# Kernel optimization log

Hardware: AMD Instinct MI355X
Metric: run time of the kernel (lower is better)

The kernel has to match this reference:

```python
import jax, jax.numpy as jnp
import numpy as np

NUM_CLASSES = 10
LAMBDA_COORD = 5.0
LAMBDA_NOOBJ = 0.5
B, S, P = 2048, 26, 5 + NUM_CLASSES


def setup_inputs() -> dict:
    key = jax.random.key(0)
    k1, k2 = jax.random.split(key)
    predictions = jax.random.normal(k1, (B, S, S, P), dtype=jnp.float32)
    targets = jax.random.normal(k2, (B, S * S * P,), dtype=jnp.float32)
    return {"predictions": predictions, "targets": targets}


def reference(predictions, targets):
    b, s, _, p = predictions.shape
    pred = predictions.reshape(b, s * s, p)          # (B, S*S, 5+C)
    tgt = targets.reshape(b, s * s, -1)              # (B, S*S, 5+C)

    obj = tgt[..., 4] > 0                            # object mask per cell

    # Coordinate loss: lambda_coord * sum((pred_xywh - tgt_xywh)^2) over object cells
    coord_sq = jnp.sum((pred[..., :4] - tgt[..., :4]) ** 2, axis=-1)
    coord_loss = LAMBDA_COORD * jnp.sum(jnp.where(obj, coord_sq, 0.0))

    # Confidence loss: (sigmoid(p_conf) - t_conf)^2 on obj cells,
    # lambda_noobj * sigmoid(p_conf)^2 on no-obj cells (scalar MSE mean == squared diff)
    conf_p = jax.nn.sigmoid(pred[..., 4])
    conf_loss = jnp.sum(jnp.where(obj,
                                  (conf_p - tgt[..., 4]) ** 2,
                                  LAMBDA_NOOBJ * conf_p ** 2))

    # Classification loss: mean over C of squared diff per object cell, summed
    cls_sq = jnp.mean((pred[..., 5:5 + NUM_CLASSES] - tgt[..., 5:5 + NUM_CLASSES]) ** 2, axis=-1)
    class_loss = jnp.sum(jnp.where(obj, cls_sq, 0.0))

    total_loss = coord_loss + conf_loss + class_loss
    return (total_loss, coord_loss, conf_loss, class_loss)
```

## Files before the change

kernel.cpp:

```cpp
#include <hip/hip_runtime.h>

constexpr int   NUM_CLASSES  = 10;
constexpr float LAMBDA_COORD = 5.0f;
constexpr float LAMBDA_NOOBJ = 0.5f;
constexpr int   BLOCK = 256;
constexpr int   NBLOCKS_MAX = 2028;
constexpr int   UNROLL = 5;

__device__ __forceinline__ void slot(const float4 p, const float4 t,
                                     const float t4a, const float t4b,
                                     unsigned j0,
                                     float& coord, float& conf, float& cls)
{
    const float pm[4] = {p.x, p.y, p.z, p.w};
    const float tm[4] = {t.x, t.y, t.z, t.w};

#pragma unroll
    for (int m = 0; m < 4; ++m) {
        unsigned j  = j0 + (unsigned)m;
        float d     = pm[m] - tm[m];
        float sq    = d * d;
        float t4    = (j >= 15u) ? t4b : t4a;
        float sqo   = (t4 > 0.f) ? sq : 0.f;
        coord += ((j - 4u) >= 11u) ? sqo : 0.f;
        cls   += ((j - 5u) <  10u) ? sqo : 0.f;
    }

    bool  hasConf = (j0 - 1u) < 4u;
    float pc = (j0 == 4u) ? pm[0]
             : (j0 == 3u) ? pm[1]
             : (j0 == 2u) ? pm[2]
             :              pm[3];
    float e   = __expf(-pc);
    float sig = 1.f / (1.f + e);
    bool  obj = t4a > 0.f;
    float dsv = sig - t4a;
    float confv = obj ? dsv * dsv : LAMBDA_NOOBJ * sig * sig;
    conf += hasConf ? confv : 0.f;
}

__global__ __launch_bounds__(BLOCK) void yolo_main(
    const float4* __restrict__ pred4,
    const float4* __restrict__ tgt4,
    const float*  __restrict__ tgt,
    float* __restrict__ ws,
    unsigned n4, unsigned nblocks)
{
    unsigned idx    = blockIdx.x * BLOCK + threadIdx.x;
    unsigned stride = nblocks * BLOCK;

    float coord = 0.f, conf = 0.f, cls = 0.f;

    unsigned k = idx;
    for (; k + (UNROLL - 1) * stride < n4; k += UNROLL * stride) {
        float4   p[UNROLL], t[UNROLL];
        float    ta[UNROLL], tb[UNROLL];
        unsigned j0s[UNROLL];

#pragma unroll
        for (int u = 0; u < UNROLL; ++u) {
            unsigned kk    = k + (unsigned)u * stride;
            p[u]           = pred4[kk];
            t[u]           = tgt4[kk];
            unsigned base  = 4u * kk;
            unsigned cell0 = base / 15u;
            unsigned c15   = cell0 * 15u;
            unsigned j0    = base - c15;
            j0s[u]         = j0;
            ta[u]          = tgt[c15 + 4u];
            tb[u]          = tgt[(j0 >= 12u) ? c15 + 19u : c15 + 4u];
        }

#pragma unroll
        for (int u = 0; u < UNROLL; ++u)
            slot(p[u], t[u], ta[u], tb[u], j0s[u], coord, conf, cls);
    }

    for (; k < n4; k += stride) {
        float4 p = pred4[k];
        float4 t = tgt4[k];
        unsigned base  = 4u * k;
        unsigned cell0 = base / 15u;
        unsigned c15   = cell0 * 15u;
        unsigned j0    = base - c15;
        float ta = tgt[c15 + 4u];
        float tb = tgt[(j0 >= 12u) ? c15 + 19u : c15 + 4u];
        slot(p, t, ta, tb, j0, coord, conf, cls);
    }

#pragma unroll
    for (int off = 32; off > 0; off >>= 1) {
        coord += __shfl_down(coord, off);
        conf  += __shfl_down(conf,  off);
        cls   += __shfl_down(cls,   off);
    }

    __shared__ float s[3][4];
    int wave = threadIdx.x >> 6, lane = threadIdx.x & 63;
    if (lane == 0) { s[0][wave] = coord; s[1][wave] = conf; s[2][wave] = cls; }
    __syncthreads();

    if (threadIdx.x == 0) {
        float c0 = s[0][0] + s[0][1] + s[0][2] + s[0][3];
        float c1 = s[1][0] + s[1][1] + s[1][2] + s[1][3];
        float c2 = s[2][0] + s[2][1] + s[2][2] + s[2][3];
        ws[blockIdx.x]               = c0;
        ws[nblocks + blockIdx.x]     = c1;
        ws[2 * nblocks + blockIdx.x] = c2;
    }
}

__global__ __launch_bounds__(BLOCK) void yolo_finalize(
    const float* __restrict__ ws, float* __restrict__ out, unsigned nblocks)
{
    float c0 = 0.f, c1 = 0.f, c2 = 0.f;
    for (unsigned i = threadIdx.x; i < nblocks; i += BLOCK) {
        c0 += ws[i];
        c1 += ws[nblocks + i];
        c2 += ws[2 * nblocks + i];
    }
#pragma unroll
    for (int off = 32; off > 0; off >>= 1) {
        c0 += __shfl_down(c0, off);
        c1 += __shfl_down(c1, off);
        c2 += __shfl_down(c2, off);
    }
    __shared__ float s[3][4];
    int wave = threadIdx.x >> 6, lane = threadIdx.x & 63;
    if (lane == 0) { s[0][wave] = c0; s[1][wave] = c1; s[2][wave] = c2; }
    __syncthreads();
    if (threadIdx.x == 0) {
        float coord = LAMBDA_COORD * (s[0][0] + s[0][1] + s[0][2] + s[0][3]);
        float conf  =                 s[1][0] + s[1][1] + s[1][2] + s[1][3];
        float cls   = (1.f / NUM_CLASSES) * (s[2][0] + s[2][1] + s[2][2] + s[2][3]);
        out[0] = coord + conf + cls;
        out[1] = coord;
        out[2] = conf;
        out[3] = cls;
    }
}

extern "C" void kernel_launch(void* const* d_in, const int* in_sizes, int n_in,
                              void* d_out, int out_size, void* d_ws, size_t ws_size,
                              hipStream_t stream) {
    const float* pred = (const float*)d_in[0];
    const float* tgt  = (const float*)d_in[1];
    float* out = (float*)d_out;
    float* ws  = (float*)d_ws;

    unsigned total = (unsigned)in_sizes[0];
    unsigned n4    = total / 4u;

    unsigned nblocks = NBLOCKS_MAX;
    size_t need = (size_t)nblocks * 3 * sizeof(float);
    if (need > ws_size) nblocks = (unsigned)(ws_size / (3 * sizeof(float)));

    yolo_main<<<nblocks, BLOCK, 0, stream>>>(
        (const float4*)pred, (const float4*)tgt, tgt, ws, n4, nblocks);
    yolo_finalize<<<1, BLOCK, 0, stream>>>(ws, out, nblocks);
}
```

Measured before the change: 185.0 us.

## Stage tiles through LDS with async global_load_lds double buffering

The grid-stride register-unrolled loop is replaced by a tile loop. Each block streams 256-float4 tiles of predictions and targets into LDS using global_load_lds, double-buffered so the next tile loads while the current one is computed. The per-cell objectness values come from the LDS target tile plus small halo regions, which removes the extra scattered global reads of tgt[c15+4]. The cost is a __syncthreads per tile, only one float4 in flight per thread instead of five, and more LDS use, which may reduce occupancy.

New measurement: 186.0 us. No clear change (+0.5%).

```diff
diff --git a/kernel.cpp b/kernel.cpp
--- a/kernel.cpp
+++ b/kernel.cpp
@@ -5,7 +5,15 @@
 constexpr float LAMBDA_NOOBJ = 0.5f;
 constexpr int   BLOCK = 256;
 constexpr int   NBLOCKS_MAX = 2028;
-constexpr int   UNROLL = 5;
+
+constexpr int LDSP_F  = 256 * 4;
+constexpr int LDST_F  = 12 + 1024 + 16;
+constexpr int LDST_FP = 1056;
+
+#define GLOAD_LDS16(gp, lp) \
+    __builtin_amdgcn_global_load_lds( \
+        (const __attribute__((address_space(1))) void*)(gp), \
+        (__attribute__((address_space(3))) void*)(lp), 16, 0, 0)
 
 __device__ __forceinline__ void slot(const float4 p, const float4 t,
                                      const float t4a, const float t4b,
@@ -46,46 +54,81 @@
     float* __restrict__ ws,
     unsigned n4, unsigned nblocks)
 {
-    unsigned idx    = blockIdx.x * BLOCK + threadIdx.x;
-    unsigned stride = nblocks * BLOCK;
+    __shared__ float ldsP[2][LDSP_F];
+    __shared__ float ldsT[2][LDST_FP];
+
+    const int tid = (int)threadIdx.x;
+    const unsigned ntiles = n4 / 256u;
 
     float coord = 0.f, conf = 0.f, cls = 0.f;
 
-    unsigned k = idx;
-    for (; k + (UNROLL - 1) * stride < n4; k += UNROLL * stride) {
-        float4   p[UNROLL], t[UNROLL];
-        float    ta[UNROLL], tb[UNROLL];
-        unsigned j0s[UNROLL];
-
-#pragma unroll
-        for (int u = 0; u < UNROLL; ++u) {
-            unsigned kk    = k + (unsigned)u * stride;
-            p[u]           = pred4[kk];
-            t[u]           = tgt4[kk];
-            unsigned base  = 4u * kk;
+    unsigned NT = (ntiles > blockIdx.x) ? ((ntiles - 1u - blockIdx.x) / nblocks + 1u) : 0u;
+
+    if (NT > 0) {
+        {
+            unsigned s0 = blockIdx.x * 256u;
+            GLOAD_LDS16(pred4 + s0 + tid, &ldsP[0][4 * tid]);
+            GLOAD_LDS16(tgt4  + s0 + tid, &ldsT[0][12 + 4 * tid]);
+            if (tid < 7) {
+                int hs = (tid < 3) ? (int)s0 - 3 + tid : (int)s0 + 253 + tid;
+                hs = hs < 0 ? 0 : hs;
+                hs = hs > (int)n4 - 1 ? (int)n4 - 1 : hs;
+                float4 hv = tgt4[hs];
+                int off = (tid < 3) ? 4 * tid : 1036 + 4 * (tid - 3);
+                *(float4*)&ldsT[0][off] = hv;
+            }
+        }
+        __syncthreads();
+
+        for (unsigned T = 0; T < NT; ++T) {
+            const int cur  = (int)(T & 1u);
+            const bool more = (T + 1u < NT);
+
+            float4 hv = make_float4(0.f, 0.f, 0.f, 0.f);
+            if (more) {
+                unsigned s0n = (blockIdx.x + (T + 1u) * nblocks) * 256u;
+                GLOAD_LDS16(pred4 + s0n + tid, &ldsP[cur ^ 1][4 * tid]);
+                GLOAD_LDS16(tgt4  + s0n + tid, &ldsT[cur ^ 1][12 + 4 * tid]);
+                if (tid < 7) {
+                    int hs = (tid < 3) ? (int)s0n - 3 + tid : (int)s0n + 253 + tid;
+                    hs = hs < 0 ? 0 : hs;
+                    hs = hs > (int)n4 - 1 ? (int)n4 - 1 : hs;
+                    hv = tgt4[hs];
+                }
+            }
+
+            {
+                unsigned s0   = (blockIdx.x + T * nblocks) * 256u;
+                float4 p = *(const float4*)&ldsP[cur][4 * tid];
+                float4 t = *(const float4*)&ldsT[cur][12 + 4 * tid];
+                unsigned base = (s0 + (unsigned)tid) * 4u;
+                unsigned j0   = base % 15u;
+                int qoff = 4 * tid + 16 - (int)j0;
+                float t4a = ldsT[cur][qoff];
+                float t4b = ldsT[cur][qoff + ((j0 >= 12u) ? 15 : 0)];
+                slot(p, t, t4a, t4b, j0, coord, conf, cls);
+            }
+
+            if (more && tid < 7) {
+                int off = (tid < 3) ? 4 * tid : 1036 + 4 * (tid - 3);
+                *(float4*)&ldsT[cur ^ 1][off] = hv;
+            }
+            __syncthreads();
+        }
+    }
+
+    if (blockIdx.x == 0) {
+        for (unsigned k = ntiles * 256u + (unsigned)tid; k < n4; k += BLOCK) {
+            float4 p = pred4[k];
+            float4 t = tgt4[k];
+            unsigned base  = 4u * k;
             unsigned cell0 = base / 15u;
             unsigned c15   = cell0 * 15u;
             unsigned j0    = base - c15;
-            j0s[u]         = j0;
-            ta[u]          = tgt[c15 + 4u];
-            tb[u]          = tgt[(j0 >= 12u) ? c15 + 19u : c15 + 4u];
+            float ta = tgt[c15 + 4u];
+            float tb = tgt[(j0 >= 12u) ? c15 + 19u : c15 + 4u];
+            slot(p, t, ta, tb, j0, coord, conf, cls);
         }
-
-#pragma unroll
-        for (int u = 0; u < UNROLL; ++u)
-            slot(p[u], t[u], ta[u], tb[u], j0s[u], coord, conf, cls);
-    }
-
-    for (; k < n4; k += stride) {
-        float4 p = pred4[k];
-        float4 t = tgt4[k];
-        unsigned base  = 4u * k;
-        unsigned cell0 = base / 15u;
-        unsigned c15   = cell0 * 15u;
-        unsigned j0    = base - c15;
-        float ta = tgt[c15 + 4u];
-        float tb = tgt[(j0 >= 12u) ? c15 + 19u : c15 + 4u];
-        slot(p, t, ta, tb, j0, coord, conf, cls);
     }
 
 #pragma unroll
@@ -96,11 +139,11 @@
     }
 
     __shared__ float s[3][4];
-    int wave = threadIdx.x >> 6, lane = threadIdx.x & 63;
+    int wave = tid >> 6, lane = tid & 63;
     if (lane == 0) { s[0][wave] = coord; s[1][wave] = conf; s[2][wave] = cls; }
     __syncthreads();
 
-    if (threadIdx.x == 0) {
+    if (tid == 0) {
         float c0 = s[0][0] + s[0][1] + s[0][2] + s[0][3];
         float c1 = s[1][0] + s[1][1] + s[1][2] + s[1][3];
         float c2 = s[2][0] + s[2][1] + s[2][2] + s[2][3];
```

## Stage target tiles into LDS via async global_load_lds with double buffering

Applied to the files above, without the earlier changes.

Replaces the unrolled register-load loop with a two-stage software pipeline. Each wave streams its slice of the target tensor into a per-wave LDS buffer using global_load_lds, plus a few halo float4 loads, and prediction loads are marked nontemporal. The per-cell objectness values (t4a/t4b) are then read from LDS instead of issuing extra scattered global loads. This removes the redundant gathers of the confidence column and overlaps the next tile's loads with the current tile's math. In exchange it adds manual waitcnt/sched_barrier control, halo-handling complexity and LDS usage that may limit occupancy.

Measured after the change: 179.5 us. -3.0%, faster.

```diff
diff --git a/kernel.cpp b/kernel.cpp
--- a/kernel.cpp
+++ b/kernel.cpp
@@ -1,36 +1,42 @@
 #include <hip/hip_runtime.h>
+
+typedef float f4v __attribute__((ext_vector_type(4)));
 
 constexpr int   NUM_CLASSES  = 10;
 constexpr float LAMBDA_COORD = 5.0f;
 constexpr float LAMBDA_NOOBJ = 0.5f;
 constexpr int   BLOCK = 256;
 constexpr int   NBLOCKS_MAX = 2028;
-constexpr int   UNROLL = 5;
-
-__device__ __forceinline__ void slot(const float4 p, const float4 t,
+constexpr int   LDST_W = 288;
+
+#define GLOAD_LDS16(gp, lp) \
+    __builtin_amdgcn_global_load_lds( \
+        (const __attribute__((address_space(1))) void*)(gp), \
+        (__attribute__((address_space(3))) void*)(lp), 16, 0, 0)
+#define WAITVM(n)  asm volatile("s_waitcnt vmcnt(" #n ")" ::: "memory")
+#define WAITLGKM() asm volatile("s_waitcnt lgkmcnt(0)" ::: "memory")
+#define SB()       __builtin_amdgcn_sched_barrier(0)
+
+__device__ __forceinline__ void slot(const f4v p, const f4v t,
                                      const float t4a, const float t4b,
                                      unsigned j0,
                                      float& coord, float& conf, float& cls)
 {
-    const float pm[4] = {p.x, p.y, p.z, p.w};
-    const float tm[4] = {t.x, t.y, t.z, t.w};
-
 #pragma unroll
     for (int m = 0; m < 4; ++m) {
         unsigned j  = j0 + (unsigned)m;
-        float d     = pm[m] - tm[m];
+        float d     = p[m] - t[m];
         float sq    = d * d;
         float t4    = (j >= 15u) ? t4b : t4a;
         float sqo   = (t4 > 0.f) ? sq : 0.f;
         coord += ((j - 4u) >= 11u) ? sqo : 0.f;
         cls   += ((j - 5u) <  10u) ? sqo : 0.f;
     }
-
     bool  hasConf = (j0 - 1u) < 4u;
-    float pc = (j0 == 4u) ? pm[0]
-             : (j0 == 3u) ? pm[1]
-             : (j0 == 2u) ? pm[2]
-             :              pm[3];
+    float pc = (j0 == 4u) ? p[0]
+             : (j0 == 3u) ? p[1]
+             : (j0 == 2u) ? p[2]
+             :              p[3];
     float e   = __expf(-pc);
     float sig = 1.f / (1.f + e);
     bool  obj = t4a > 0.f;
@@ -39,52 +45,102 @@
     conf += hasConf ? confv : 0.f;
 }
 
+#define STAGE(LBUF, TT, PREG, HREG) do {                                     \
+    unsigned kk_ = idx + (unsigned)(TT) * S;                                 \
+    PREG = __builtin_nontemporal_load((const f4v*)pred4 + kk_);              \
+    GLOAD_LDS16((const f4v*)tgt4 + kk_, (LBUF) + 12 + 4 * lane);             \
+    if (lane < 7u) {                                                         \
+        int kw_ = (int)(kk_ - lane);                                         \
+        int hs_ = (lane < 3u) ? kw_ - 3 + (int)lane : kw_ + 61 + (int)lane;  \
+        hs_ = hs_ < 0 ? 0 : hs_;                                             \
+        hs_ = hs_ > (int)n4 - 1 ? (int)n4 - 1 : hs_;                         \
+        HREG = *((const f4v*)tgt4 + hs_);                                    \
+    }                                                                        \
+} while (0)
+
+#define CLOAD(LBUF, TT, HREG, TV, AV, BV, JV) do {                           \
+    if (lane < 7u) {                                                         \
+        int off_ = (lane < 3u) ? 4 * (int)lane : 268 + 4 * ((int)lane - 3);  \
+        *(f4v*)((LBUF) + off_) = HREG;                                       \
+    }                                                                        \
+    unsigned kk_ = idx + (unsigned)(TT) * S;                                 \
+    JV = (4u * kk_) % 15u;                                                   \
+    int q_ = 4 * (int)lane + 16 - (int)JV;                                   \
+    TV = *(const f4v*)((LBUF) + 12 + 4 * lane);                              \
+    AV = (LBUF)[q_];                                                         \
+    BV = (LBUF)[q_ + ((JV >= 12u) ? 15 : 0)];                                \
+} while (0)
+
 __global__ __launch_bounds__(BLOCK) void yolo_main(
-    const float4* __restrict__ pred4,
-    const float4* __restrict__ tgt4,
-    const float*  __restrict__ tgt,
+    const float* __restrict__ pred4,
+    const float* __restrict__ tgt4,
     float* __restrict__ ws,
     unsigned n4, unsigned nblocks)
 {
-    unsigned idx    = blockIdx.x * BLOCK + threadIdx.x;
-    unsigned stride = nblocks * BLOCK;
+    __shared__ float ldsT[4][2][LDST_W];
+
+    const unsigned tid  = threadIdx.x;
+    const unsigned lane = tid & 63u;
+    const unsigned wv   = tid >> 6;
+    const unsigned S    = nblocks * 256u;
+    const unsigned idx  = blockIdx.x * 256u + tid;
+    const unsigned NTu  = n4 / S;
+
+    float* L0 = &ldsT[wv][0][0];
+    float* L1 = &ldsT[wv][1][0];
 
     float coord = 0.f, conf = 0.f, cls = 0.f;
-
-    unsigned k = idx;
-    for (; k + (UNROLL - 1) * stride < n4; k += UNROLL * stride) {
-        float4   p[UNROLL], t[UNROLL];
-        float    ta[UNROLL], tb[UNROLL];
-        unsigned j0s[UNROLL];
-
-#pragma unroll
-        for (int u = 0; u < UNROLL; ++u) {
-            unsigned kk    = k + (unsigned)u * stride;
-            p[u]           = pred4[kk];
-            t[u]           = tgt4[kk];
-            unsigned base  = 4u * kk;
-            unsigned cell0 = base / 15u;
-            unsigned c15   = cell0 * 15u;
-            unsigned j0    = base - c15;
-            j0s[u]         = j0;
-            ta[u]          = tgt[c15 + 4u];
-            tb[u]          = tgt[(j0 >= 12u) ? c15 + 19u : c15 + 4u];
+    f4v pA = {0,0,0,0}, pB = {0,0,0,0}, hA = {0,0,0,0}, hB = {0,0,0,0};
+
+    if (NTu >= 2u) {
+        STAGE(L0, 0, pA, hA); SB();
+        STAGE(L1, 1, pB, hB); SB();
+        unsigned T = 0;
+        for (; T + 1u < NTu; T += 2u) {
+            WAITVM(3); SB();
+            f4v tA; float aA, bA; unsigned jA;
+            CLOAD(L0, T, hA, tA, aA, bA, jA);
+            WAITLGKM(); SB();
+            f4v puA = pA;
+            if (T + 2u < NTu) { STAGE(L0, T + 2u, pA, hA); }
+            SB();
+            slot(puA, tA, aA, bA, jA, coord, conf, cls);
+
+            if (T + 2u < NTu) { WAITVM(3); } else { WAITVM(0); }
+            SB();
+            f4v tB; float aB, bB; unsigned jB;
+            CLOAD(L1, T + 1u, hB, tB, aB, bB, jB);
+            WAITLGKM(); SB();
+            f4v puB = pB;
+            if (T + 3u < NTu) { STAGE(L1, T + 3u, pB, hB); }
+            SB();
+            slot(puB, tB, aB, bB, jB, coord, conf, cls);
         }
-
-#pragma unroll
-        for (int u = 0; u < UNROLL; ++u)
-            slot(p[u], t[u], ta[u], tb[u], j0s[u], coord, conf, cls);
-    }
-
-    for (; k < n4; k += stride) {
-        float4 p = pred4[k];
-        float4 t = tgt4[k];
+        if (T < NTu) {
+            WAITVM(0); SB();
+            f4v tA; float aA, bA; unsigned jA;
+            CLOAD(L0, T, hA, tA, aA, bA, jA);
+            WAITLGKM(); SB();
+            slot(pA, tA, aA, bA, jA, coord, conf, cls);
+        }
+    } else if (NTu == 1u) {
+        STAGE(L0, 0, pA, hA); SB();
+        WAITVM(0); SB();
+        f4v tA; float aA, bA; unsigned jA;
+        CLOAD(L0, 0, hA, tA, aA, bA, jA);
+        WAITLGKM(); SB();
+        slot(pA, tA, aA, bA, jA, coord, conf, cls);
+    }
+
+    for (unsigned k = NTu * S + idx; k < n4; k += S) {
+        f4v p = *((const f4v*)pred4 + k);
+        f4v t = *((const f4v*)tgt4 + k);
         unsigned base  = 4u * k;
         unsigned cell0 = base / 15u;
         unsigned c15   = cell0 * 15u;
         unsigned j0    = base - c15;
-        float ta = tgt[c15 + 4u];
-        float tb = tgt[(j0 >= 12u) ? c15 + 19u : c15 + 4u];
+        float ta = tgt4[c15 + 4u];
+        float tb = tgt4[(j0 >= 12u) ? c15 + 19u : c15 + 4u];
         slot(p, t, ta, tb, j0, coord, conf, cls);
     }
 
@@ -96,11 +152,10 @@
     }
 
     __shared__ float s[3][4];
-    int wave = threadIdx.x >> 6, lane = threadIdx.x & 63;
-    if (lane == 0) { s[0][wave] = coord; s[1][wave] = conf; s[2][wave] = cls; }
+    if (lane == 0) { s[0][wv] = coord; s[1][wv] = conf; s[2][wv] = cls; }
     __syncthreads();
 
-    if (threadIdx.x == 0) {
+    if (tid == 0) {
         float c0 = s[0][0] + s[0][1] + s[0][2] + s[0][3];
         float c1 = s[1][0] + s[1][1] + s[1][2] + s[1][3];
         float c2 = s[2][0] + s[2][1] + s[2][2] + s[2][3];
@@ -155,7 +210,6 @@
     size_t need = (size_t)nblocks * 3 * sizeof(float);
     if (need > ws_size) nblocks = (unsigned)(ws_size / (3 * sizeof(float)));
 
-    yolo_main<<<nblocks, BLOCK, 0, stream>>>(
-        (const float4*)pred, (const float4*)tgt, tgt, ws, n4, nblocks);
+    yolo_main<<<nblocks, BLOCK, 0, stream>>>(pred, tgt, ws, n4, nblocks);
     yolo_finalize<<<1, BLOCK, 0, stream>>>(ws, out, nblocks);
 }
```
